# Performance work log

Measured on AMD Instinct MI355X. Metric: run time of the kernel, lower is better.

Reference implementation:

```python
import jax, jax.numpy as jnp
import numpy as np

B, H, W, C = 8, 64, 64, 256  # NHWC, SAGAN-style feature map


def setup_inputs() -> dict:
    key = jax.random.key(0)
    ks = jax.random.split(key, 10)
    d_qk, d_v = C // 8, C // 2
    sc = lambda fan_in: 1.0 / np.sqrt(fan_in)
    return {
        "x": jax.random.normal(ks[0], (B, H, W, C), dtype=jnp.float32),
        "Wf": jax.random.normal(ks[1], (C, d_qk), dtype=jnp.float32) * sc(C),
        "bf": jnp.zeros((d_qk,), dtype=jnp.float32),
        "Wg": jax.random.normal(ks[2], (C, d_qk), dtype=jnp.float32) * sc(C),
        "bg": jnp.zeros((d_qk,), dtype=jnp.float32),
        "Wh": jax.random.normal(ks[3], (C, d_v), dtype=jnp.float32) * sc(C),
        "bh": jnp.zeros((d_v,), dtype=jnp.float32),
        "Wo": jax.random.normal(ks[4], (d_v, C), dtype=jnp.float32) * sc(d_v),
        "bo": jnp.zeros((C,), dtype=jnp.float32),
        # original inits gamma=0.0 (identity fwd); use nonzero so fwd exercises attention
        "gamma": jnp.float32(0.5),
    }


def reference(x, Wf, bf, Wg, bg, Wh, bh, Wo, bo, gamma):
    b, h_, w_, c = x.shape
    n = h_ * w_
    xf = x.reshape(b, n, c)  # 1x1 convs are per-pixel GEMMs
    f = xf @ Wf + bf          # [B, N, C/8]  (keys)
    g = xf @ Wg + bg          # [B, N, C/8]  (queries)
    hv = xf @ Wh + bh         # [B, N, C/2]  (values)
    s = jnp.einsum('bnd,bmd->bnm', g, f)   # unscaled scores [B, N, N]
    beta = jax.nn.softmax(s, axis=-1)
    o = jnp.einsum('bnm,bmd->bnd', beta, hv)  # [B, N, C/2]
    o = o @ Wo + bo                           # output 1x1 conv -> [B, N, C]
    out = gamma * o + xf
    return out.reshape(b, h_, w_, c)
```

## Files before the change

### kernel.cpp

```cpp
#include <hip/hip_runtime.h>
#include <hip/hip_bf16.h>

#define NB   8
#define CC   256
#define NN   4096
#define NTOT (NB*NN)
#define DQK  32
#define DV   128

typedef __attribute__((ext_vector_type(8))) short bf16x8;
typedef __attribute__((ext_vector_type(4))) float f32x4;
typedef __attribute__((ext_vector_type(16))) float f32x16;
typedef __attribute__((ext_vector_type(4))) float float4v;
typedef __attribute__((ext_vector_type(4))) unsigned int u32x4;

__device__ __forceinline__ short f2bf(float f) {
    __hip_bfloat16 h = __float2bfloat16(f);
    return *reinterpret_cast<short*>(&h);
}
__device__ __forceinline__ float bf2f(short s) {
    unsigned int u = ((unsigned int)(unsigned short)s) << 16;
    return __builtin_bit_cast(float, u);
}
__device__ __forceinline__ unsigned int cvtpk(float lo, float hi) {
    unsigned int r;
    asm("v_cvt_pk_bf16_f32 %0, %1, %2" : "=v"(r) : "v"(lo), "v"(hi));
    return r;
}
__device__ __forceinline__ void plswap(unsigned int &a, unsigned int &b) {
    asm("v_permlane32_swap_b32 %0, %1" : "+v"(a), "+v"(b));
}

#define OFF_F     0u
#define OFF_G     (2u<<20)
#define OFF_HVT   (4u<<20)
#define OFF_OP    (12u<<20)
#define OFF_LS    (28u<<20)
#define OFF_WQKVT ((28u<<20)+(512u<<10))
#define OFF_WOT   (OFF_WQKVT + 192u*256u*2u)

__global__ __launch_bounds__(256) void prep_kernel(
    const float* __restrict__ Wf, const float* __restrict__ Wg,
    const float* __restrict__ Wh, const float* __restrict__ Wo,
    short* __restrict__ WqkvT, short* __restrict__ WoT)
{
    int idx = blockIdx.x * 256 + threadIdx.x;
    if (idx < 192 * 256) {
        int j = idx >> 8, k = idx & 255;
        float v = (j < 32) ? Wf[k * 32 + j]
                : (j < 64) ? Wg[k * 32 + (j - 32)]
                           : Wh[k * 128 + (j - 64)];
        WqkvT[j * 256 + k] = f2bf(v);
    }
    int i2 = idx - 192 * 256;
    if (i2 >= 0 && i2 < 256 * 128) {
        int c = i2 >> 7, d = i2 & 127;
        WoT[c * 128 + d] = f2bf(Wo[d * 256 + c]);
    }
}

__global__ __launch_bounds__(256) void proj_kernel(
    const float* __restrict__ x,
    const float* __restrict__ bf_, const float* __restrict__ bg_,
    const float* __restrict__ bh_,
    const short* __restrict__ WqkvT,
    short* __restrict__ fws, short* __restrict__ gws, short* __restrict__ hvT)
{
    int wid = threadIdx.x >> 6, lane = threadIdx.x & 63;
    int col16 = lane & 15, rq = lane >> 4;
    int rbase = blockIdx.x * 64 + wid * 16;
    int arow = rbase + col16;

    f32x4 acc[12];
    #pragma unroll
    for (int i = 0; i < 12; ++i) acc[i] = (f32x4){0.f, 0.f, 0.f, 0.f};

    const float* xrow = x + (size_t)arow * CC;
    #pragma unroll
    for (int kk = 0; kk < 8; ++kk) {
        int k0 = kk * 32 + rq * 8;
        float4v u0 = *(const float4v*)(xrow + k0);
        float4v u1 = *(const float4v*)(xrow + k0 + 4);
        bf16x8 av;
        av[0]=f2bf(u0[0]); av[1]=f2bf(u0[1]); av[2]=f2bf(u0[2]); av[3]=f2bf(u0[3]);
        av[4]=f2bf(u1[0]); av[5]=f2bf(u1[1]); av[6]=f2bf(u1[2]); av[7]=f2bf(u1[3]);
        #pragma unroll
        for (int nf = 0; nf < 12; ++nf) {
            bf16x8 bv = *(const bf16x8*)(WqkvT + (nf * 16 + col16) * 256 + k0);
            acc[nf] = __builtin_amdgcn_mfma_f32_16x16x32_bf16(av, bv, acc[nf], 0, 0, 0);
        }
    }

    #pragma unroll
    for (int nf = 0; nf < 12; ++nf) {
        int colg = nf * 16 + col16;
        #pragma unroll
        for (int r = 0; r < 4; ++r) {
            int rowg = rbase + rq * 4 + r;
            float val = acc[nf][r];
            if (colg < 32) {
                fws[(size_t)rowg * DQK + colg] = f2bf(val + bf_[colg]);
            } else if (colg < 64) {
                int c = colg - 32;
                gws[(size_t)rowg * DQK + c] = f2bf((val + bg_[c]) * 1.44269504089f);
            } else {
                int d = colg - 64;
                int b = rowg >> 12, n = rowg & 4095;
                hvT[((size_t)(b * DV + d)) * NN + n] = f2bf(val + bh_[d]);
            }
        }
    }
}

__global__ __launch_bounds__(256) void attn_kernel(
    const short* __restrict__ fws, const short* __restrict__ gws,
    const short* __restrict__ hvT, short* __restrict__ opart,
    float* __restrict__ lspart)
{
    __shared__ __align__(16) char smem[33280];

    int t = threadIdx.x;
    int wid = t >> 6, lane = t & 63;
    int l31 = lane & 31, lh = lane >> 5;
    int qh = wid >> 1, kh = wid & 1;

    int bid = blockIdx.x;
    int sid = (bid & 7) * 128 + (bid >> 3);
    int b = sid >> 7, rem = sid & 127;
    int ksh = rem >> 6, qt = rem & 63;
    int qbase = b * NN + qt * 64;
    int k0 = ksh * 32, kend = k0 + 32;

    const short* grow = gws + (size_t)(qbase + qh * 32 + l31) * DQK;
    bf16x8 gb0 = *(const bf16x8*)(grow + lh * 8);
    bf16x8 gb1 = *(const bf16x8*)(grow + 16 + lh * 8);

    int d0 = t >> 3, j0 = t & 7;
    int row0 = d0 >> 1;
    int vldsoff0 = row0 * 256 + (((((d0 & 1) << 3) | j0) ^ (row0 & 15)) << 4);
    const short* vbase = hvT + ((size_t)(b * DV + d0)) * NN + j0 * 8;

    const short* fbase = fws + (size_t)(b * NN + kh * 32 + l31) * DQK + lh * 8;

    {
        bf16x8 v0 = *(const bf16x8*)(vbase + (size_t)k0 * 64);
        bf16x8 v1 = *(const bf16x8*)(vbase + 1u * 32 * NN + (size_t)k0 * 64);
        bf16x8 v2 = *(const bf16x8*)(vbase + 2u * 32 * NN + (size_t)k0 * 64);
        bf16x8 v3 = *(const bf16x8*)(vbase + 3u * 32 * NN + (size_t)k0 * 64);
        *(bf16x8*)(&smem[vldsoff0])         = v0;
        *(bf16x8*)(&smem[vldsoff0 + 4096])  = v1;
        *(bf16x8*)(&smem[vldsoff0 + 8192])  = v2;
        *(bf16x8*)(&smem[vldsoff0 + 12288]) = v3;
    }
    bf16x8 fc0 = *(const bf16x8*)(fbase + (size_t)k0 * 2048);
    bf16x8 fc1 = *(const bf16x8*)(fbase + (size_t)k0 * 2048 + 16);
    __syncthreads();

    f32x16 oacc[4], zero16;
    #pragma unroll
    for (int i = 0; i < 16; ++i) {
        zero16[i] = 0.f;
        oacc[0][i] = 0.f; oacc[1][i] = 0.f; oacc[2][i] = 0.f; oacc[3][i] = 0.f;
    }
    float lsum = 0.f;

    int cur = 0;
    for (int kb = k0; kb < kend; ++kb) {
        int kbn = (kb + 1 < kend) ? kb + 1 : kb;
        bf16x8 vn0 = *(const bf16x8*)(vbase + (size_t)kbn * 64);
        bf16x8 vn1 = *(const bf16x8*)(vbase + 1u * 32 * NN + (size_t)kbn * 64);
        bf16x8 vn2 = *(const bf16x8*)(vbase + 2u * 32 * NN + (size_t)kbn * 64);
        bf16x8 vn3 = *(const bf16x8*)(vbase + 3u * 32 * NN + (size_t)kbn * 64);
        bf16x8 fn0 = *(const bf16x8*)(fbase + (size_t)kbn * 2048);
        bf16x8 fn1 = *(const bf16x8*)(fbase + (size_t)kbn * 2048 + 16);

        f32x16 s = __builtin_amdgcn_mfma_f32_32x32x16_bf16(fc0, gb0, zero16, 0, 0, 0);
        s = __builtin_amdgcn_mfma_f32_32x32x16_bf16(fc1, gb1, s, 0, 0, 0);

        unsigned int w[8];
        #pragma unroll
        for (int i = 0; i < 8; ++i) {
            float pa = __builtin_exp2f(s[2 * i]);
            float pb = __builtin_exp2f(s[2 * i + 1]);
            lsum += pa + pb;
            w[i] = cvtpk(pa, pb);
        }
        plswap(w[0], w[2]); plswap(w[1], w[3]);
        plswap(w[4], w[6]); plswap(w[5], w[7]);

        const char* bufc = &smem[cur * 16384];
        #pragma unroll
        for (int ks = 0; ks < 2; ++ks) {
            u32x4 pw = { w[ks * 4], w[ks * 4 + 1], w[ks * 4 + 2], w[ks * 4 + 3] };
            bf16x8 pa = __builtin_bit_cast(bf16x8, pw);
            int kslot = kh * 2 + ks;
            #pragma unroll
            for (int dt = 0; dt < 4; ++dt) {
                int d = dt * 32 + l31;
                int vrow = d >> 1;
                int vch = ((((d & 1) << 3) | (kslot * 2 + lh)) ^ (vrow & 15));
                bf16x8 vb = *(const bf16x8*)(bufc + vrow * 256 + vch * 16);
                oacc[dt] = __builtin_amdgcn_mfma_f32_32x32x16_bf16(pa, vb, oacc[dt], 0, 0, 0);
            }
        }

        char* bufn = &smem[(cur ^ 1) * 16384];
        *(bf16x8*)(bufn + vldsoff0)         = vn0;
        *(bf16x8*)(bufn + vldsoff0 + 4096)  = vn1;
        *(bf16x8*)(bufn + vldsoff0 + 8192)  = vn2;
        *(bf16x8*)(bufn + vldsoff0 + 12288) = vn3;
        __syncthreads();
        cur ^= 1;
        fc0 = fn0; fc1 = fn1;
    }

    float lt = lsum + __shfl_xor(lsum, 32);
    float* lsbuf = (float*)(&smem[32768]);
    if (lh == 0) lsbuf[(qh * 2 + kh) * 32 + l31] = lt;
    float* obuf = (float*)(&smem[qh * 16384]);
    if (kh == 1) {
        #pragma unroll
        for (int dt = 0; dt < 4; ++dt) {
            #pragma unroll
            for (int c = 0; c < 4; ++c) {
                f32x4 ch = { oacc[dt][4 * c], oacc[dt][4 * c + 1],
                             oacc[dt][4 * c + 2], oacc[dt][4 * c + 3] };
                *(f32x4*)&obuf[lane * 64 + (((dt * 4 + c) ^ (lane & 15)) << 2)] = ch;
            }
        }
    }
    __syncthreads();
    if (kh == 0) {
        float ltb = lsbuf[qh * 64 + l31] + lsbuf[qh * 64 + 32 + l31];
        if (lh == 0) lspart[(size_t)(qbase + qh * 32 + l31) * 2 + ksh] = ltb;
        float inv = 1.f / ltb;
        #pragma unroll
        for (int dt = 0; dt < 4; ++dt) {
            f32x4 pc[4];
            #pragma unroll
            for (int c = 0; c < 4; ++c)
                pc[c] = *(const f32x4*)&obuf[lane * 64 + (((dt * 4 + c) ^ (lane & 15)) << 2)];
            #pragma unroll
            for (int r = 0; r < 16; ++r) {
                float val = oacc[dt][r] + pc[r >> 2][r & 3];
                int qr = (r & 3) + 8 * (r >> 2) + 4 * lh;
                float iv = __shfl(inv, qr);
                opart[((size_t)(qbase + qh * 32 + qr) * 2 + ksh) * 128 + dt * 32 + l31]
                    = f2bf(val * iv);
            }
        }
    }
}

__global__ __launch_bounds__(256) void out_kernel(
    const short* __restrict__ opart, const float* __restrict__ lspart,
    const short* __restrict__ WoT,
    const float* __restrict__ bo, const float* __restrict__ gamma,
    const float* __restrict__ x, float* __restrict__ out)
{
    int wid = threadIdx.x >> 6, lane = threadIdx.x & 63;
    int col16 = lane & 15, rq = lane >> 4;
    int rbase = blockIdx.x * 64 + wid * 16;
    int arow = rbase + col16;

    float l0 = lspart[(size_t)arow * 2];
    float l1 = lspart[(size_t)arow * 2 + 1];
    float iv = 1.f / (l0 + l1);
    float w0 = l0 * iv, w1 = l1 * iv;

    const short* oprow = opart + (size_t)arow * 256;
    bf16x8 afr[4];
    #pragma unroll
    for (int kk = 0; kk < 4; ++kk) {
        bf16x8 a0 = *(const bf16x8*)(oprow + kk * 32 + rq * 8);
        bf16x8 a1 = *(const bf16x8*)(oprow + 128 + kk * 32 + rq * 8);
        bf16x8 af;
        #pragma unroll
        for (int j = 0; j < 8; ++j)
            af[j] = f2bf(w0 * bf2f(a0[j]) + w1 * bf2f(a1[j]));
        afr[kk] = af;
    }

    f32x4 acc[16];
    #pragma unroll
    for (int i = 0; i < 16; ++i) acc[i] = (f32x4){0.f, 0.f, 0.f, 0.f};

    #pragma unroll
    for (int nf = 0; nf < 16; ++nf) {
        #pragma unroll
        for (int kk = 0; kk < 4; ++kk) {
            bf16x8 bfr = *(const bf16x8*)(WoT + (nf * 16 + col16) * DV + kk * 32 + rq * 8);
            acc[nf] = __builtin_amdgcn_mfma_f32_16x16x32_bf16(afr[kk], bfr, acc[nf], 0, 0, 0);
        }
    }

    float gm = gamma[0];
    #pragma unroll
    for (int nf = 0; nf < 16; ++nf) {
        int colg = nf * 16 + col16;
        float bov = bo[colg];
        #pragma unroll
        for (int r = 0; r < 4; ++r) {
            int rowg = rbase + rq * 4 + r;
            out[(size_t)rowg * CC + colg] = gm * (acc[nf][r] + bov) + x[(size_t)rowg * CC + colg];
        }
    }
}

extern "C" void kernel_launch(void* const* d_in, const int* in_sizes, int n_in,
                              void* d_out, int out_size, void* d_ws, size_t ws_size,
                              hipStream_t stream)
{
    const float* x     = (const float*)d_in[0];
    const float* Wf    = (const float*)d_in[1];
    const float* bf_   = (const float*)d_in[2];
    const float* Wg    = (const float*)d_in[3];
    const float* bg_   = (const float*)d_in[4];
    const float* Wh    = (const float*)d_in[5];
    const float* bh_   = (const float*)d_in[6];
    const float* Wo    = (const float*)d_in[7];
    const float* bo    = (const float*)d_in[8];
    const float* gamma = (const float*)d_in[9];

    char* ws = (char*)d_ws;
    short* fws   = (short*)(ws + OFF_F);
    short* gws   = (short*)(ws + OFF_G);
    short* hvT   = (short*)(ws + OFF_HVT);
    short* opart = (short*)(ws + OFF_OP);
    float* lsp   = (float*)(ws + OFF_LS);
    short* WqkvT = (short*)(ws + OFF_WQKVT);
    short* WoT   = (short*)(ws + OFF_WOT);
    float* out   = (float*)d_out;

    hipLaunchKernelGGL(prep_kernel, dim3(320), dim3(256), 0, stream, Wf, Wg, Wh, Wo, WqkvT, WoT);
    hipLaunchKernelGGL(proj_kernel, dim3(512), dim3(256), 0, stream,
                       x, bf_, bg_, bh_, WqkvT, fws, gws, hvT);
    hipLaunchKernelGGL(attn_kernel, dim3(1024), dim3(256), 0, stream, fws, gws, hvT, opart, lsp);
    hipLaunchKernelGGL(out_kernel, dim3(512), dim3(256), 0, stream, opart, lsp, WoT, bo, gamma, x, out);
}
```

Measured before the change: 149.7 us.

## Pre-tile V in MFMA fragment layout and read directly from global

The projection kernel now writes V in a tiled layout that matches the MFMA operand fragment, so the attention loop loads V fragments straight from global memory. This removes the LDS double-buffer staging and the per-iteration __syncthreads. The PV MFMA is transposed so V is the A operand. The epilogue is reworked to combine the two key halves in LDS and write bf16 output with vectorized stores. Launch bounds now request 4 blocks per CU. The trade-off is more global/L2 traffic per wave, since every wave reloads V, in exchange for no barriers. The last loop iteration also reads f one tile past the end of its range.

```diff
diff --git a/kernel.cpp b/kernel.cpp
--- a/kernel.cpp
+++ b/kernel.cpp
@@ -33,7 +33,7 @@
 
 #define OFF_F     0u
 #define OFF_G     (2u<<20)
-#define OFF_HVT   (4u<<20)
+#define OFF_VT    (4u<<20)
 #define OFF_OP    (12u<<20)
 #define OFF_LS    (28u<<20)
 #define OFF_WQKVT ((28u<<20)+(512u<<10))
@@ -64,7 +64,7 @@
     const float* __restrict__ bf_, const float* __restrict__ bg_,
     const float* __restrict__ bh_,
     const short* __restrict__ WqkvT,
-    short* __restrict__ fws, short* __restrict__ gws, short* __restrict__ hvT)
+    short* __restrict__ fws, short* __restrict__ gws, short* __restrict__ vtile)
 {
     int wid = threadIdx.x >> 6, lane = threadIdx.x & 63;
     int col16 = lane & 15, rq = lane >> 4;
@@ -106,15 +106,18 @@
             } else {
                 int d = colg - 64;
                 int b = rowg >> 12, n = rowg & 4095;
-                hvT[((size_t)(b * DV + d)) * NN + n] = f2bf(val + bh_[d]);
+                int kt = n >> 6, kslot = (n >> 4) & 3, klh = (n >> 3) & 1, j = n & 7;
+                size_t addr = (((size_t)(b * 64 + kt) * 4 + kslot) * 2048)
+                            + (d >> 5) * 512 + klh * 256 + (d & 31) * 8 + j;
+                vtile[addr] = f2bf(val + bh_[d]);
             }
         }
     }
 }
 
-__global__ __launch_bounds__(256) void attn_kernel(
+__global__ __launch_bounds__(256, 4) void attn_kernel(
     const short* __restrict__ fws, const short* __restrict__ gws,
-    const short* __restrict__ hvT, short* __restrict__ opart,
+    const short* __restrict__ vtile, short* __restrict__ opart,
     float* __restrict__ lspart)
 {
     __shared__ __align__(16) char smem[33280];
@@ -135,44 +138,23 @@
     bf16x8 gb0 = *(const bf16x8*)(grow + lh * 8);
     bf16x8 gb1 = *(const bf16x8*)(grow + 16 + lh * 8);
 
-    int d0 = t >> 3, j0 = t & 7;
-    int row0 = d0 >> 1;
-    int vldsoff0 = row0 * 256 + (((((d0 & 1) << 3) | j0) ^ (row0 & 15)) << 4);
-    const short* vbase = hvT + ((size_t)(b * DV + d0)) * NN + j0 * 8;
-
-    const short* fbase = fws + (size_t)(b * NN + kh * 32 + l31) * DQK + lh * 8;
-
-    {
-        bf16x8 v0 = *(const bf16x8*)(vbase + (size_t)k0 * 64);
-        bf16x8 v1 = *(const bf16x8*)(vbase + 1u * 32 * NN + (size_t)k0 * 64);
-        bf16x8 v2 = *(const bf16x8*)(vbase + 2u * 32 * NN + (size_t)k0 * 64);
-        bf16x8 v3 = *(const bf16x8*)(vbase + 3u * 32 * NN + (size_t)k0 * 64);
-        *(bf16x8*)(&smem[vldsoff0])         = v0;
-        *(bf16x8*)(&smem[vldsoff0 + 4096])  = v1;
-        *(bf16x8*)(&smem[vldsoff0 + 8192])  = v2;
-        *(bf16x8*)(&smem[vldsoff0 + 12288]) = v3;
-    }
-    bf16x8 fc0 = *(const bf16x8*)(fbase + (size_t)k0 * 2048);
-    bf16x8 fc1 = *(const bf16x8*)(fbase + (size_t)k0 * 2048 + 16);
-    __syncthreads();
-
-    f32x16 oacc[4], zero16;
+    int foff = (kh * 32 + l31) * DQK + lh * 8;
+    const short* fS = fws + (size_t)b * NN * DQK;
+    bf16x8 fc0 = *(const bf16x8*)(fS + (size_t)k0 * 2048 + foff);
+    bf16x8 fc1 = *(const bf16x8*)(fS + (size_t)k0 * 2048 + foff + 16);
+
+    f32x16 oaccT[4], zero16;
     #pragma unroll
     for (int i = 0; i < 16; ++i) {
         zero16[i] = 0.f;
-        oacc[0][i] = 0.f; oacc[1][i] = 0.f; oacc[2][i] = 0.f; oacc[3][i] = 0.f;
+        oaccT[0][i] = 0.f; oaccT[1][i] = 0.f; oaccT[2][i] = 0.f; oaccT[3][i] = 0.f;
     }
     float lsum = 0.f;
 
-    int cur = 0;
     for (int kb = k0; kb < kend; ++kb) {
-        int kbn = (kb + 1 < kend) ? kb + 1 : kb;
-        bf16x8 vn0 = *(const bf16x8*)(vbase + (size_t)kbn * 64);
-        bf16x8 vn1 = *(const bf16x8*)(vbase + 1u * 32 * NN + (size_t)kbn * 64);
-        bf16x8 vn2 = *(const bf16x8*)(vbase + 2u * 32 * NN + (size_t)kbn * 64);
-        bf16x8 vn3 = *(const bf16x8*)(vbase + 3u * 32 * NN + (size_t)kbn * 64);
-        bf16x8 fn0 = *(const bf16x8*)(fbase + (size_t)kbn * 2048);
-        bf16x8 fn1 = *(const bf16x8*)(fbase + (size_t)kbn * 2048 + 16);
+        const short* fnp = fS + (size_t)(kb + 1) * 2048 + foff;
+        bf16x8 fn0 = *(const bf16x8*)(fnp);
+        bf16x8 fn1 = *(const bf16x8*)(fnp + 16);
 
         f32x16 s = __builtin_amdgcn_mfma_f32_32x32x16_bf16(fc0, gb0, zero16, 0, 0, 0);
         s = __builtin_amdgcn_mfma_f32_32x32x16_bf16(fc1, gb1, s, 0, 0, 0);
@@ -188,66 +170,69 @@
         plswap(w[0], w[2]); plswap(w[1], w[3]);
         plswap(w[4], w[6]); plswap(w[5], w[7]);
 
-        const char* bufc = &smem[cur * 16384];
+        const short* vb_kb = vtile + (((size_t)(b * 64 + kb) * 4 + kh * 2) * 2048)
+                           + (size_t)lane * 8;
         #pragma unroll
         for (int ks = 0; ks < 2; ++ks) {
             u32x4 pw = { w[ks * 4], w[ks * 4 + 1], w[ks * 4 + 2], w[ks * 4 + 3] };
-            bf16x8 pa = __builtin_bit_cast(bf16x8, pw);
-            int kslot = kh * 2 + ks;
+            bf16x8 pb_ = __builtin_bit_cast(bf16x8, pw);
             #pragma unroll
             for (int dt = 0; dt < 4; ++dt) {
-                int d = dt * 32 + l31;
-                int vrow = d >> 1;
-                int vch = ((((d & 1) << 3) | (kslot * 2 + lh)) ^ (vrow & 15));
-                bf16x8 vb = *(const bf16x8*)(bufc + vrow * 256 + vch * 16);
-                oacc[dt] = __builtin_amdgcn_mfma_f32_32x32x16_bf16(pa, vb, oacc[dt], 0, 0, 0);
+                bf16x8 va = *(const bf16x8*)(vb_kb + ks * 2048 + dt * 512);
+                oaccT[dt] = __builtin_amdgcn_mfma_f32_32x32x16_bf16(va, pb_, oaccT[dt], 0, 0, 0);
             }
         }
-
-        char* bufn = &smem[(cur ^ 1) * 16384];
-        *(bf16x8*)(bufn + vldsoff0)         = vn0;
-        *(bf16x8*)(bufn + vldsoff0 + 4096)  = vn1;
-        *(bf16x8*)(bufn + vldsoff0 + 8192)  = vn2;
-        *(bf16x8*)(bufn + vldsoff0 + 12288) = vn3;
-        __syncthreads();
-        cur ^= 1;
         fc0 = fn0; fc1 = fn1;
     }
 
-    float lt = lsum + __shfl_xor(lsum, 32);
+    lsum += __shfl_xor(lsum, 32);
     float* lsbuf = (float*)(&smem[32768]);
-    if (lh == 0) lsbuf[(qh * 2 + kh) * 32 + l31] = lt;
-    float* obuf = (float*)(&smem[qh * 16384]);
+    if (lh == 0) lsbuf[(qh * 2 + kh) * 32 + l31] = lsum;
+    __syncthreads();
+
+    char* obuf = smem;
     if (kh == 1) {
         #pragma unroll
         for (int dt = 0; dt < 4; ++dt) {
             #pragma unroll
-            for (int c = 0; c < 4; ++c) {
-                f32x4 ch = { oacc[dt][4 * c], oacc[dt][4 * c + 1],
-                             oacc[dt][4 * c + 2], oacc[dt][4 * c + 3] };
-                *(f32x4*)&obuf[lane * 64 + (((dt * 4 + c) ^ (lane & 15)) << 2)] = ch;
+            for (int r = 0; r < 16; ++r) {
+                int d = dt * 32 + (r & 3) + 8 * (r >> 2) + 4 * lh;
+                int q = qh * 32 + l31;
+                int byte = q * 512 + ((((d >> 2) ^ (q & 31)) << 4) | ((d & 3) << 2));
+                *(float*)(obuf + byte) = oaccT[dt][r];
             }
         }
     }
     __syncthreads();
     if (kh == 0) {
-        float ltb = lsbuf[qh * 64 + l31] + lsbuf[qh * 64 + 32 + l31];
-        if (lh == 0) lspart[(size_t)(qbase + qh * 32 + l31) * 2 + ksh] = ltb;
-        float inv = 1.f / ltb;
+        float tot = lsbuf[qh * 64 + l31] + lsbuf[qh * 64 + 32 + l31];
+        if (lh == 0) lspart[(size_t)(qbase + qh * 32 + l31) * 2 + ksh] = tot;
+        float iv = 1.f / tot;
         #pragma unroll
         for (int dt = 0; dt < 4; ++dt) {
-            f32x4 pc[4];
-            #pragma unroll
-            for (int c = 0; c < 4; ++c)
-                pc[c] = *(const f32x4*)&obuf[lane * 64 + (((dt * 4 + c) ^ (lane & 15)) << 2)];
             #pragma unroll
             for (int r = 0; r < 16; ++r) {
-                float val = oacc[dt][r] + pc[r >> 2][r & 3];
-                int qr = (r & 3) + 8 * (r >> 2) + 4 * lh;
-                float iv = __shfl(inv, qr);
-                opart[((size_t)(qbase + qh * 32 + qr) * 2 + ksh) * 128 + dt * 32 + l31]
-                    = f2bf(val * iv);
+                int d = dt * 32 + (r & 3) + 8 * (r >> 2) + 4 * lh;
+                int q = qh * 32 + l31;
+                int byte = q * 512 + ((((d >> 2) ^ (q & 31)) << 4) | ((d & 3) << 2));
+                float* p = (float*)(obuf + byte);
+                *p = (*p + oaccT[dt][r]) * iv;
             }
+        }
+    }
+    __syncthreads();
+    {
+        int q = t >> 2, dg = t & 3;
+        size_t orow = ((size_t)(qbase + q) * 2 + ksh) * 128 + dg * 32;
+        #pragma unroll
+        for (int cc = 0; cc < 8; cc += 2) {
+            int c0 = dg * 8 + cc;
+            f32x4 u0 = *(const f32x4*)(obuf + q * 512 + (((c0 ^ (q & 31)) << 4)));
+            f32x4 u1 = *(const f32x4*)(obuf + q * 512 + ((((c0 + 1) ^ (q & 31)) << 4)));
+            bf16x8 ov;
+            ov[0]=f2bf(u0[0]); ov[1]=f2bf(u0[1]); ov[2]=f2bf(u0[2]); ov[3]=f2bf(u0[3]);
+            ov[4]=f2bf(u1[0]); ov[5]=f2bf(u1[1]); ov[6]=f2bf(u1[2]); ov[7]=f2bf(u1[3]);
+            *(bf16x8*)(opart + orow + cc * 4) = ov;
         }
     }
 }
@@ -325,7 +310,7 @@
     char* ws = (char*)d_ws;
     short* fws   = (short*)(ws + OFF_F);
     short* gws   = (short*)(ws + OFF_G);
-    short* hvT   = (short*)(ws + OFF_HVT);
+    short* vtile = (short*)(ws + OFF_VT);
     short* opart = (short*)(ws + OFF_OP);
     float* lsp   = (float*)(ws + OFF_LS);
     short* WqkvT = (short*)(ws + OFF_WQKVT);
@@ -334,7 +319,7 @@
 
     hipLaunchKernelGGL(prep_kernel, dim3(320), dim3(256), 0, stream, Wf, Wg, Wh, Wo, WqkvT, WoT);
     hipLaunchKernelGGL(proj_kernel, dim3(512), dim3(256), 0, stream,
-                       x, bf_, bg_, bh_, WqkvT, fws, gws, hvT);
-    hipLaunchKernelGGL(attn_kernel, dim3(1024), dim3(256), 0, stream, fws, gws, hvT, opart, lsp);
+                       x, bf_, bg_, bh_, WqkvT, fws, gws, vtile);
+    hipLaunchKernelGGL(attn_kernel, dim3(1024), dim3(256), 0, stream, fws, gws, vtile, opart, lsp);
     hipLaunchKernelGGL(out_kernel, dim3(512), dim3(256), 0, stream, opart, lsp, WoT, bo, gamma, x, out);
 }
```

Measured after the change: 139.3 us. 1.07x faster.
